# Optimization experiments

Measured on AMD Instinct MI355X. Metric: run time of the kernel, lower is better.

## Reference

```python
import jax, jax.numpy as jnp
import numpy as np

H, DQ, DK, DV, DM = 16, 64, 64, 64, 1024
NEG = -1.0e12


def setup_inputs() -> dict:
    key = jax.random.key(0)
    ks = jax.random.split(key, 16)
    B, S = 4, 1024
    s = 0.02
    inp = {
        "query": jax.random.normal(ks[0], (B, S, DM), jnp.float32),
        "key": jax.random.normal(ks[1], (B, S, DM), jnp.float32),
        "value": jax.random.normal(ks[2], (B, S, DM), jnp.float32),
        "mask": jax.random.randint(ks[3], (B, S), 0, 2, jnp.int32),
        "Wq": jax.random.normal(ks[4], (H * DQ, DM), jnp.float32) * s,
        "bq": jnp.zeros((H * DQ,), jnp.float32),
        "Wk": jax.random.normal(ks[5], (H * DK, DM), jnp.float32) * s,
        "bk": jnp.zeros((H * DK,), jnp.float32),
        "Wv": jax.random.normal(ks[6], (H * DV, DM), jnp.float32) * s,
        "bv": jnp.zeros((H * DV,), jnp.float32),
        "Wo": jax.random.normal(ks[7], (DM, H * DV), jnp.float32) * s,
        "bo": jnp.zeros((DM,), jnp.float32),
        "ln_g": jnp.ones((DM,), jnp.float32),
        "ln_b": jnp.zeros((DM,), jnp.float32),
    }
    return inp


def _attention(query, key, value, mask, Wq, bq, Wk, bk, Wv, bv, Wo, bo, ln_g, ln_b):
    B, qL, _ = query.shape
    kL = key.shape[1]
    mf = mask.astype(jnp.float32)  # [B, kL] ; 1 = masked token
    # padding mask broadcast over query rows, then self-attn: masked query rows fully masked
    m = jnp.broadcast_to(mf[:, None, :], (B, qL, kL))
    m = jnp.where(mf[:, :, None] > 0, 1.0, m)  # [B, q, k]

    def proj(x, W, b, d):
        # [B,S,DM] -> [H,B,S,d]
        return (x @ W.T + b).reshape(B, -1, H, d).transpose(2, 0, 1, 3)

    q = proj(query, Wq, bq, DQ)
    k = proj(key, Wk, bk, DK)
    v = proj(value, Wv, bv, DV)

    scores = jnp.einsum("hbqd,hbkd->hbqk", q, k) / np.float32(np.sqrt(DK))
    fut = jnp.triu(jnp.ones((qL, kL), jnp.float32), k=1)  # [q,k] future mask
    scores = scores + m[None] * NEG + fut[None, None] * NEG
    attn = jax.nn.softmax(scores, axis=-1)
    attn = attn * (1.0 - m[None]) * (1.0 - fut[None, None])

    out = jnp.einsum("hbqk,hbkd->hbqd", attn, v)  # [H,B,q,DV]
    out = out.transpose(1, 2, 0, 3).reshape(B, qL, H * DV)
    out = out @ Wo.T + bo + query  # residual
    mu = jnp.mean(out, axis=-1, keepdims=True)
    var = jnp.mean(jnp.square(out - mu), axis=-1, keepdims=True)
    out = (out - mu) * jax.lax.rsqrt(var + 1e-12) * ln_g + ln_b
    return out, attn.reshape(H * B, qL, kL)


def reference(query, key, value, mask, Wq, bq, Wk, bk, Wv, bv, Wo, bo, ln_g, ln_b):
    return _attention(query, key, value, mask, Wq, bq, Wk, bk, Wv, bv, Wo, bo, ln_g, ln_b)
```

## Files before the change

### kernel.cpp

```cpp
#include <hip/hip_runtime.h>
#include <hip/hip_bf16.h>

typedef __attribute__((ext_vector_type(4))) float f32x4;
typedef __attribute__((ext_vector_type(4))) float fv4;
typedef __attribute__((ext_vector_type(8))) short bf16x8;
typedef __attribute__((ext_vector_type(4))) short bf16x4;

#define DEVI __device__ __forceinline__

constexpr int BATCH = 4, SEQ = 1024, NH = 16, HD = 64, DM_ = 1024;
constexpr int NTOK = BATCH * SEQ;

DEVI unsigned short f2bf(float f) {
  union { float f; unsigned u; } v; v.f = f;
  unsigned r = v.u + 0x7FFFu + ((v.u >> 16) & 1u);
  return (unsigned short)(r >> 16);
}

DEVI int swz64(int row, int col) {
  int byte = (row * 64 + col) * 2;
  byte ^= (row & 7) << 4;
  return byte >> 1;
}

DEVI void gld_lds16(const unsigned short* g, unsigned short* l) {
  __builtin_amdgcn_global_load_lds(
      (const __attribute__((address_space(1))) unsigned int*)g,
      (__attribute__((address_space(3))) unsigned int*)l, 16, 0, 0);
}

__global__ __launch_bounds__(256) void k_cvt(
    const float* __restrict__ q, const float* __restrict__ k,
    const float* __restrict__ v,
    const float* __restrict__ wq, const float* __restrict__ wk,
    const float* __restrict__ wv, const float* __restrict__ wo,
    unsigned short* __restrict__ Xb, unsigned short* __restrict__ Wb)
{
  const int a = blockIdx.y;
  const float* src;
  unsigned short* dst;
  int n;
  if (a < 3) {
    src = (a == 0) ? q : (a == 1) ? k : v;
    dst = Xb + (size_t)a * NTOK * DM_;
    n = NTOK * DM_;
  } else {
    src = (a == 3) ? wq : (a == 4) ? wk : (a == 5) ? wv : wo;
    dst = Wb + (size_t)(a - 3) * DM_ * DM_;
    n = DM_ * DM_;
  }
  const int idx = (blockIdx.x * 256 + threadIdx.x) * 8;
  if (idx >= n) return;
  fv4 v0 = *(const fv4*)(src + idx);
  fv4 v1 = *(const fv4*)(src + idx + 4);
  bf16x8 o;
  o[0] = (short)f2bf(v0[0]); o[1] = (short)f2bf(v0[1]);
  o[2] = (short)f2bf(v0[2]); o[3] = (short)f2bf(v0[3]);
  o[4] = (short)f2bf(v1[0]); o[5] = (short)f2bf(v1[1]);
  o[6] = (short)f2bf(v1[2]); o[7] = (short)f2bf(v1[3]);
  *(bf16x8*)(dst + idx) = o;
}

__global__ __launch_bounds__(256) void k_proj(
    const unsigned short* __restrict__ Xb, const unsigned short* __restrict__ Wb,
    const float* __restrict__ bq, const float* __restrict__ bk,
    const float* __restrict__ bv,
    unsigned short* __restrict__ qo, unsigned short* __restrict__ ko,
    unsigned short* __restrict__ vTo)
{
  const int z = blockIdx.z;
  const unsigned short* X = Xb + (size_t)z * NTOK * DM_;
  const unsigned short* W = Wb + (size_t)z * DM_ * DM_;
  const float* bias = (z == 0) ? bq : (z == 1) ? bk : bv;

  __shared__ __align__(16) unsigned short Al[2][64 * 64];
  __shared__ __align__(16) unsigned short Bl[2][128 * 64];

  const int tid = threadIdx.x;
  const int lane = tid & 63;
  const int w = tid >> 6;
  const int wm = w & 1, wn = w >> 1;
  const int l15 = lane & 15, lg = lane >> 4;
  const int m0 = blockIdx.x * 64;
  const int o0 = blockIdx.y * 128;

  const int rseg = lane >> 3;
  const int cg = (lane & 7) ^ rseg;

  f32x4 acc[2][4];
#pragma unroll
  for (int i = 0; i < 2; ++i)
#pragma unroll
    for (int j = 0; j < 4; ++j) acc[i][j] = f32x4{0.f, 0.f, 0.f, 0.f};

#define PROJ_STAGE(nb, kt)                                                     \
  {                                                                            \
    const int k0_ = (kt) * 64;                                                 \
    _Pragma("unroll") for (int i = 0; i < 2; ++i) {                            \
      const int seg = w * 2 + i;                                               \
      gld_lds16(X + (size_t)(m0 + seg * 8 + rseg) * DM_ + k0_ + cg * 8,        \
                &Al[nb][seg * 512]);                                           \
    }                                                                          \
    _Pragma("unroll") for (int i = 0; i < 4; ++i) {                            \
      const int seg = w * 4 + i;                                               \
      gld_lds16(W + (size_t)(o0 + seg * 8 + rseg) * DM_ + k0_ + cg * 8,        \
                &Bl[nb][seg * 512]);                                           \
    }                                                                          \
  }

  PROJ_STAGE(0, 0);
  __syncthreads();

  for (int kt = 0; kt < 16; ++kt) {
    const int cur = kt & 1;
    if (kt < 15) PROJ_STAGE(cur ^ 1, kt + 1);
#pragma unroll
    for (int kk = 0; kk < 2; ++kk) {
      bf16x8 af[2], bfm[4];
#pragma unroll
      for (int m = 0; m < 2; ++m)
        af[m] = *(const bf16x8*)&Al[cur][swz64(wm * 32 + m * 16 + l15, kk * 32 + lg * 8)];
#pragma unroll
      for (int n = 0; n < 4; ++n)
        bfm[n] = *(const bf16x8*)&Bl[cur][swz64(wn * 64 + n * 16 + l15, kk * 32 + lg * 8)];
#pragma unroll
      for (int m = 0; m < 2; ++m)
#pragma unroll
        for (int n = 0; n < 4; ++n)
          acc[m][n] = __builtin_amdgcn_mfma_f32_16x16x32_bf16(af[m], bfm[n], acc[m][n], 0, 0, 0);
    }
    __syncthreads();
  }

#pragma unroll
  for (int n = 0; n < 4; ++n) {
    const int oc = o0 + wn * 64 + n * 16 + l15;
    const float bb = bias[oc];
#pragma unroll
    for (int m = 0; m < 2; ++m) {
      const int rbase = m0 + wm * 32 + m * 16 + lg * 4;
      if (z == 2) {
        bf16x4 pv;
#pragma unroll
        for (int j = 0; j < 4; ++j) pv[j] = (short)f2bf(acc[m][n][j] + bb);
        *(bf16x4*)&vTo[((size_t)(rbase >> 10) * 1024 + oc) * 1024 + (rbase & 1023)] = pv;
      } else {
        unsigned short* Y = (z == 0) ? qo : ko;
        const float sc = (z == 0) ? 0.125f : 1.f;
#pragma unroll
        for (int j = 0; j < 4; ++j)
          Y[(size_t)(rbase + j) * DM_ + oc] = f2bf((acc[m][n][j] + bb) * sc);
      }
    }
  }
}

__global__ __launch_bounds__(512, 2) void k_attn_pv(
    const unsigned short* __restrict__ qb, const unsigned short* __restrict__ kb,
    const unsigned short* __restrict__ vT, const int* __restrict__ mask,
    float* __restrict__ attn, unsigned short* __restrict__ Ob)
{
  const int tid = threadIdx.x;
  const int lane = tid & 63;
  const int w = tid >> 6;
  const int l15 = lane & 15, lg = lane >> 4;
  const int hb = blockIdx.y;
  const int h = hb >> 2, b = hb & 3;
  const int bx = blockIdx.x;
  const int q0 = bx * 32;

  __shared__ __align__(16) unsigned short Pl[32 * 1024];
  __shared__ float red[8][2][16];

  int qglob[2];
  qglob[0] = q0 + l15;
  qglob[1] = q0 + 16 + l15;

  bf16x8 qf[2][2];
#pragma unroll
  for (int g = 0; g < 2; ++g) {
    const unsigned short* qp = qb + (size_t)(b * SEQ + qglob[g]) * DM_ + h * HD + lg * 8;
    qf[g][0] = *(const bf16x8*)qp;
    qf[g][1] = *(const bf16x8*)(qp + 32);
  }
  int qm[2];
  qm[0] = mask[b * SEQ + qglob[0]];
  qm[1] = mask[b * SEQ + qglob[1]];

  const int tt = 2 * bx + 1;
  const int ni = (tt >= w) ? ((tt - w) >> 3) + 1 : 0;

  bf16x8 kf[8][2];
#pragma unroll
  for (int i = 0; i < 8; ++i) {
    if (i < ni) {
      const int krow = (w + 8 * i) * 16 + l15;
      const unsigned short* kp = kb + (size_t)(b * SEQ + krow) * DM_ + h * HD + lg * 8;
      kf[i][0] = *(const bf16x8*)kp;
      kf[i][1] = *(const bf16x8*)(kp + 32);
    }
  }

  f32x4 acc[8][2];
#pragma unroll
  for (int i = 0; i < 8; ++i)
#pragma unroll
    for (int g = 0; g < 2; ++g) acc[i][g] = f32x4{0.f, 0.f, 0.f, 0.f};

#pragma unroll
  for (int i = 0; i < 8; ++i) {
    if (i < ni) {
#pragma unroll
      for (int g = 0; g < 2; ++g) {
        acc[i][g] = __builtin_amdgcn_mfma_f32_16x16x32_bf16(kf[i][0], qf[g][0], acc[i][g], 0, 0, 0);
        acc[i][g] = __builtin_amdgcn_mfma_f32_16x16x32_bf16(kf[i][1], qf[g][1], acc[i][g], 0, 0, 0);
      }
    }
  }

  unsigned kvb = 0;
#pragma unroll
  for (int i = 0; i < 8; ++i) {
    if (i < ni) {
      const int kbase = (w + 8 * i) * 16 + lg * 4;
      int4 mv = *(const int4*)&mask[b * SEQ + kbase];
      if (mv.x == 0) kvb |= 1u << (i * 4 + 0);
      if (mv.y == 0) kvb |= 1u << (i * 4 + 1);
      if (mv.z == 0) kvb |= 1u << (i * 4 + 2);
      if (mv.w == 0) kvb |= 1u << (i * 4 + 3);
    }
  }

  float s[2] = {0.f, 0.f};
#pragma unroll
  for (int i = 0; i < 8; ++i) {
    if (i < ni) {
      const int kbase = (w + 8 * i) * 16 + lg * 4;
#pragma unroll
      for (int j = 0; j < 4; ++j) {
        const bool kok = (kvb >> (i * 4 + j)) & 1u;
#pragma unroll
        for (int g = 0; g < 2; ++g) {
          const bool vld = kok && (qm[g] == 0) && (kbase + j <= qglob[g]);
          const float p = vld ? __expf(acc[i][g][j]) : 0.f;
          acc[i][g][j] = p;
          s[g] += p;
        }
      }
    }
  }
#pragma unroll
  for (int g = 0; g < 2; ++g) {
    s[g] += __shfl_xor(s[g], 16, 64);
    s[g] += __shfl_xor(s[g], 32, 64);
  }
  if (lane < 16) { red[w][0][l15] = s[0]; red[w][1][l15] = s[1]; }
  __syncthreads();
  float rinv[2];
#pragma unroll
  for (int g = 0; g < 2; ++g) {
    float sm = 0.f;
#pragma unroll
    for (int ww = 0; ww < 8; ++ww) sm += red[ww][g][l15];
    rinv[g] = (sm > 0.f) ? (1.f / sm) : 0.f;
  }

#pragma unroll
  for (int i = 0; i < 8; ++i) {
    const int kbase = (w + 8 * i) * 16 + lg * 4;
#pragma unroll
    for (int g = 0; g < 2; ++g) {
      float* ap = attn + (size_t)hb * SEQ * SEQ + (size_t)qglob[g] * SEQ;
      fv4 st = fv4{0.f, 0.f, 0.f, 0.f};
      bf16x4 pb = bf16x4{0, 0, 0, 0};
      if (i < ni) {
#pragma unroll
        for (int j = 0; j < 4; ++j) {
          st[j] = acc[i][g][j] * rinv[g];
          pb[j] = (short)f2bf(acc[i][g][j]);
        }
      }
      __builtin_nontemporal_store(st, (fv4*)&ap[kbase]);
      const int row = g * 16 + l15;
      const int pbyte = ((row * 1024 + kbase) * 2) ^ ((l15 & 7) << 4);
      *(bf16x4*)((char*)Pl + pbyte) = pb;
    }
  }
  __syncthreads();

  const int dt = w & 3, g = w >> 2;
  const int prow = g * 16 + l15;
  f32x4 o = f32x4{0.f, 0.f, 0.f, 0.f};
  const unsigned short* vr = vT + (size_t)(b * 1024 + h * HD + dt * 16 + l15) * 1024;
#pragma unroll 4
  for (int kt = 0; kt <= bx; ++kt) {
    const int k0 = kt * 32 + lg * 8;
    bf16x8 vf = *(const bf16x8*)(vr + k0);
    const int pbyte = ((prow * 1024 + k0) * 2) ^ ((l15 & 7) << 4);
    bf16x8 pf = *(const bf16x8*)((const char*)Pl + pbyte);
    o = __builtin_amdgcn_mfma_f32_16x16x32_bf16(vf, pf, o, 0, 0, 0);
  }

  bf16x4 ob;
#pragma unroll
  for (int j = 0; j < 4; ++j) ob[j] = (short)f2bf(o[j] * rinv[g]);
  *(bf16x4*)&Ob[(size_t)(b * SEQ + q0 + prow) * DM_ + h * HD + dt * 16 + lg * 4] = ob;
}

__global__ __launch_bounds__(256) void k_oproj(
    const unsigned short* __restrict__ Ob, const unsigned short* __restrict__ Wb,
    const float* __restrict__ bo, const float* __restrict__ query,
    float* __restrict__ preln)
{
  const unsigned short* W = Wb + (size_t)3 * DM_ * DM_;

  __shared__ __align__(16) unsigned short Al[2][64 * 64];
  __shared__ __align__(16) unsigned short Bl[2][128 * 64];

  const int tid = threadIdx.x;
  const int lane = tid & 63;
  const int w = tid >> 6;
  const int wm = w & 1, wn = w >> 1;
  const int l15 = lane & 15, lg = lane >> 4;
  const int m0 = blockIdx.x * 64;
  const int o0 = blockIdx.y * 128;

  const int rseg = lane >> 3;
  const int cg = (lane & 7) ^ rseg;

  f32x4 acc[2][4];
#pragma unroll
  for (int i = 0; i < 2; ++i)
#pragma unroll
    for (int j = 0; j < 4; ++j) acc[i][j] = f32x4{0.f, 0.f, 0.f, 0.f};

#define OPROJ_STAGE(nb, kt)                                                    \
  {                                                                            \
    const int k0_ = (kt) * 64;                                                 \
    _Pragma("unroll") for (int i = 0; i < 2; ++i) {                            \
      const int seg = w * 2 + i;                                               \
      gld_lds16(Ob + (size_t)(m0 + seg * 8 + rseg) * DM_ + k0_ + cg * 8,       \
                &Al[nb][seg * 512]);                                           \
    }                                                                          \
    _Pragma("unroll") for (int i = 0; i < 4; ++i) {                            \
      const int seg = w * 4 + i;                                               \
      gld_lds16(W + (size_t)(o0 + seg * 8 + rseg) * DM_ + k0_ + cg * 8,        \
                &Bl[nb][seg * 512]);                                           \
    }                                                                          \
  }

  OPROJ_STAGE(0, 0);
  __syncthreads();

  for (int kt = 0; kt < 16; ++kt) {
    const int cur = kt & 1;
    if (kt < 15) OPROJ_STAGE(cur ^ 1, kt + 1);
#pragma unroll
    for (int kk = 0; kk < 2; ++kk) {
      bf16x8 af[2], bfm[4];
#pragma unroll
      for (int m = 0; m < 2; ++m)
        af[m] = *(const bf16x8*)&Al[cur][swz64(wm * 32 + m * 16 + l15, kk * 32 + lg * 8)];
#pragma unroll
      for (int n = 0; n < 4; ++n)
        bfm[n] = *(const bf16x8*)&Bl[cur][swz64(wn * 64 + n * 16 + l15, kk * 32 + lg * 8)];
#pragma unroll
      for (int m = 0; m < 2; ++m)
#pragma unroll
        for (int n = 0; n < 4; ++n)
          acc[m][n] = __builtin_amdgcn_mfma_f32_16x16x32_bf16(af[m], bfm[n], acc[m][n], 0, 0, 0);
    }
    __syncthreads();
  }

#pragma unroll
  for (int n = 0; n < 4; ++n) {
    const int oc = o0 + wn * 64 + n * 16 + l15;
    const float bb = bo[oc];
#pragma unroll
    for (int m = 0; m < 2; ++m) {
      const int rbase = m0 + wm * 32 + m * 16 + lg * 4;
#pragma unroll
      for (int j = 0; j < 4; ++j) {
        const size_t idx = (size_t)(rbase + j) * DM_ + oc;
        preln[idx] = acc[m][n][j] + bb + query[idx];
      }
    }
  }
}

__global__ __launch_bounds__(256) void k_ln(
    const float* __restrict__ x, const float* __restrict__ g,
    const float* __restrict__ bta, float* __restrict__ out)
{
  const int row = blockIdx.x;
  const int tid = threadIdx.x;
  const float* xr = x + (size_t)row * DM_;
  fv4 v = *(const fv4*)(xr + tid * 4);
  float s = v[0] + v[1] + v[2] + v[3];
  float s2 = v[0] * v[0] + v[1] * v[1] + v[2] * v[2] + v[3] * v[3];
#pragma unroll
  for (int off = 1; off < 64; off <<= 1) {
    s += __shfl_xor(s, off, 64);
    s2 += __shfl_xor(s2, off, 64);
  }
  __shared__ float rs[2][4];
  const int w = tid >> 6;
  if ((tid & 63) == 0) { rs[0][w] = s; rs[1][w] = s2; }
  __syncthreads();
  s = rs[0][0] + rs[0][1] + rs[0][2] + rs[0][3];
  s2 = rs[1][0] + rs[1][1] + rs[1][2] + rs[1][3];
  const float mu = s * (1.f / 1024.f);
  const float var = s2 * (1.f / 1024.f) - mu * mu;
  const float rstd = rsqrtf(var + 1e-12f);
  fv4 gg = *(const fv4*)(g + tid * 4);
  fv4 bb = *(const fv4*)(bta + tid * 4);
  fv4 o;
#pragma unroll
  for (int j = 0; j < 4; ++j) o[j] = (v[j] - mu) * rstd * gg[j] + bb[j];
  *(fv4*)(out + (size_t)row * DM_ + tid * 4) = o;
}

extern "C" void kernel_launch(void* const* d_in, const int* in_sizes, int n_in,
                              void* d_out, int out_size, void* d_ws, size_t ws_size,
                              hipStream_t stream) {
  const float* query = (const float*)d_in[0];
  const float* key   = (const float*)d_in[1];
  const float* value = (const float*)d_in[2];
  const int*   mask  = (const int*)d_in[3];
  const float* Wq = (const float*)d_in[4];
  const float* bq = (const float*)d_in[5];
  const float* Wk = (const float*)d_in[6];
  const float* bk = (const float*)d_in[7];
  const float* Wv = (const float*)d_in[8];
  const float* bv = (const float*)d_in[9];
  const float* Wo = (const float*)d_in[10];
  const float* bo = (const float*)d_in[11];
  const float* ln_g = (const float*)d_in[12];
  const float* ln_b = (const float*)d_in[13];

  float* out  = (float*)d_out;
  float* attn = out + (size_t)NTOK * DM_;

  char* ws = (char*)d_ws;
  unsigned short* Xb = (unsigned short*)ws;
  unsigned short* Wb = Xb + (size_t)3 * NTOK * DM_;
  unsigned short* qb = Wb + (size_t)4 * DM_ * DM_;
  unsigned short* kb = qb + (size_t)NTOK * DM_;
  unsigned short* vT = kb + (size_t)NTOK * DM_;
  unsigned short* Ob = vT + (size_t)NTOK * DM_;
  float* preln = (float*)ws;

  k_cvt<<<dim3(2048, 7), 256, 0, stream>>>(query, key, value, Wq, Wk, Wv, Wo,
                                           Xb, Wb);
  k_proj<<<dim3(64, 8, 3), 256, 0, stream>>>(Xb, Wb, bq, bk, bv, qb, kb, vT);
  k_attn_pv<<<dim3(32, 64), 512, 0, stream>>>(qb, kb, vT, mask, attn, Ob);
  k_oproj<<<dim3(64, 8), 256, 0, stream>>>(Ob, Wb, bo, query, preln);
  k_ln<<<4096, 256, 0, stream>>>(preln, ln_g, ln_b, out);
}
```

Measured before the change: 507.9 us.

## Enlarge QKV projection tile to 128x128 with swizzled 1D grid, single-buffered LDS

```diff
diff --git a/kernel.cpp b/kernel.cpp
--- a/kernel.cpp
+++ b/kernel.cpp
@@ -61,95 +61,87 @@
   *(bf16x8*)(dst + idx) = o;
 }
 
-__global__ __launch_bounds__(256) void k_proj(
+__global__ __launch_bounds__(256, 3) void k_proj(
     const unsigned short* __restrict__ Xb, const unsigned short* __restrict__ Wb,
     const float* __restrict__ bq, const float* __restrict__ bk,
     const float* __restrict__ bv,
     unsigned short* __restrict__ qo, unsigned short* __restrict__ ko,
     unsigned short* __restrict__ vTo)
 {
-  const int z = blockIdx.z;
+  const int lid = blockIdx.x;
+  const int wg = (lid & 7) * 96 + (lid >> 3);
+  const int m0 = (wg & 31) * 128;
+  const int o0g = (wg >> 5) * 128;
+  const int z = o0g >> 10;
+  const int o0 = o0g & 1023;
+
   const unsigned short* X = Xb + (size_t)z * NTOK * DM_;
-  const unsigned short* W = Wb + (size_t)z * DM_ * DM_;
   const float* bias = (z == 0) ? bq : (z == 1) ? bk : bv;
 
-  __shared__ __align__(16) unsigned short Al[2][64 * 64];
-  __shared__ __align__(16) unsigned short Bl[2][128 * 64];
+  __shared__ __align__(16) unsigned short Al[128 * 64];
+  __shared__ __align__(16) unsigned short Bl[128 * 64];
 
   const int tid = threadIdx.x;
   const int lane = tid & 63;
   const int w = tid >> 6;
   const int wm = w & 1, wn = w >> 1;
   const int l15 = lane & 15, lg = lane >> 4;
-  const int m0 = blockIdx.x * 64;
-  const int o0 = blockIdx.y * 128;
 
   const int rseg = lane >> 3;
   const int cg = (lane & 7) ^ rseg;
 
-  f32x4 acc[2][4];
-#pragma unroll
-  for (int i = 0; i < 2; ++i)
+  f32x4 acc[4][4];
+#pragma unroll
+  for (int i = 0; i < 4; ++i)
 #pragma unroll
     for (int j = 0; j < 4; ++j) acc[i][j] = f32x4{0.f, 0.f, 0.f, 0.f};
 
-#define PROJ_STAGE(nb, kt)                                                     \
-  {                                                                            \
-    const int k0_ = (kt) * 64;                                                 \
-    _Pragma("unroll") for (int i = 0; i < 2; ++i) {                            \
-      const int seg = w * 2 + i;                                               \
-      gld_lds16(X + (size_t)(m0 + seg * 8 + rseg) * DM_ + k0_ + cg * 8,        \
-                &Al[nb][seg * 512]);                                           \
-    }                                                                          \
-    _Pragma("unroll") for (int i = 0; i < 4; ++i) {                            \
-      const int seg = w * 4 + i;                                               \
-      gld_lds16(W + (size_t)(o0 + seg * 8 + rseg) * DM_ + k0_ + cg * 8,        \
-                &Bl[nb][seg * 512]);                                           \
-    }                                                                          \
-  }
-
-  PROJ_STAGE(0, 0);
-  __syncthreads();
-
   for (int kt = 0; kt < 16; ++kt) {
-    const int cur = kt & 1;
-    if (kt < 15) PROJ_STAGE(cur ^ 1, kt + 1);
+    const int k0 = kt * 64;
+    __syncthreads();
+#pragma unroll
+    for (int i = 0; i < 4; ++i) {
+      const int seg = w * 4 + i;
+      const int row = seg * 8 + rseg;
+      gld_lds16(X + (size_t)(m0 + row) * DM_ + k0 + cg * 8, &Al[seg * 512]);
+      gld_lds16(Wb + (size_t)(o0g + row) * DM_ + k0 + cg * 8, &Bl[seg * 512]);
+    }
+    __syncthreads();
 #pragma unroll
     for (int kk = 0; kk < 2; ++kk) {
-      bf16x8 af[2], bfm[4];
-#pragma unroll
-      for (int m = 0; m < 2; ++m)
-        af[m] = *(const bf16x8*)&Al[cur][swz64(wm * 32 + m * 16 + l15, kk * 32 + lg * 8)];
+      bf16x8 af[4], bfm[4];
+#pragma unroll
+      for (int m = 0; m < 4; ++m)
+        af[m] = *(const bf16x8*)&Al[swz64(wm * 64 + m * 16 + l15, kk * 32 + lg * 8)];
 #pragma unroll
       for (int n = 0; n < 4; ++n)
-        bfm[n] = *(const bf16x8*)&Bl[cur][swz64(wn * 64 + n * 16 + l15, kk * 32 + lg * 8)];
-#pragma unroll
-      for (int m = 0; m < 2; ++m)
+        bfm[n] = *(const bf16x8*)&Bl[swz64(wn * 64 + n * 16 + l15, kk * 32 + lg * 8)];
+#pragma unroll
+      for (int m = 0; m < 4; ++m)
 #pragma unroll
         for (int n = 0; n < 4; ++n)
           acc[m][n] = __builtin_amdgcn_mfma_f32_16x16x32_bf16(af[m], bfm[n], acc[m][n], 0, 0, 0);
     }
-    __syncthreads();
   }
 
 #pragma unroll
   for (int n = 0; n < 4; ++n) {
-    const int oc = o0 + wn * 64 + n * 16 + l15;
-    const float bb = bias[oc];
-#pragma unroll
-    for (int m = 0; m < 2; ++m) {
-      const int rbase = m0 + wm * 32 + m * 16 + lg * 4;
+    const int colg = o0 + wn * 64 + n * 16 + l15;
+    const float bb = bias[colg];
+#pragma unroll
+    for (int m = 0; m < 4; ++m) {
+      const int rbase = m0 + wm * 64 + m * 16 + lg * 4;
       if (z == 2) {
         bf16x4 pv;
 #pragma unroll
         for (int j = 0; j < 4; ++j) pv[j] = (short)f2bf(acc[m][n][j] + bb);
-        *(bf16x4*)&vTo[((size_t)(rbase >> 10) * 1024 + oc) * 1024 + (rbase & 1023)] = pv;
+        *(bf16x4*)&vTo[((size_t)(rbase >> 10) * 1024 + colg) * 1024 + (rbase & 1023)] = pv;
       } else {
         unsigned short* Y = (z == 0) ? qo : ko;
         const float sc = (z == 0) ? 0.125f : 1.f;
 #pragma unroll
         for (int j = 0; j < 4; ++j)
-          Y[(size_t)(rbase + j) * DM_ + oc] = f2bf((acc[m][n][j] + bb) * sc);
+          Y[(size_t)(rbase + j) * DM_ + colg] = f2bf((acc[m][n][j] + bb) * sc);
       }
     }
   }
@@ -453,7 +445,7 @@
 
   k_cvt<<<dim3(2048, 7), 256, 0, stream>>>(query, key, value, Wq, Wk, Wv, Wo,
                                            Xb, Wb);
-  k_proj<<<dim3(64, 8, 3), 256, 0, stream>>>(Xb, Wb, bq, bk, bv, qb, kb, vT);
+  k_proj<<<768, 256, 0, stream>>>(Xb, Wb, bq, bk, bv, qb, kb, vT);
   k_attn_pv<<<dim3(32, 64), 512, 0, stream>>>(qb, kb, vT, mask, attn, Ob);
   k_oproj<<<dim3(64, 8), 256, 0, stream>>>(Ob, Wb, bo, query, preln);
   k_ln<<<4096, 256, 0, stream>>>(preln, ln_g, ln_b, out);
```

Measured after the change: 499.1 us. No clear change (-1.7%).
